# Optimization experiments

Measured on AMD Instinct MI355X. Metric: run time of the kernel, lower is better.

## Reference

```python
import jax, jax.numpy as jnp
import numpy as np

EPS = 1e-12  # F.normalize default eps (denominator = max(norm, eps))


def setup_inputs() -> dict:
    key = jax.random.key(0)
    ks = jax.random.split(key, 8)
    B, FIN, H, W = 4, 256, 64, 64
    N_MEM, SQ = 64, 16           # sqrt_fin = fin**0.5
    POS_CH = 2                    # PosEncoding concatenates one coord channel per dim
    CIN = FIN + POS_CH
    QK = N_MEM * SQ               # 1024
    # PosEncoding buffer: normalized coordinate grid in [-1, 1], shape [2, H, W]
    ys = jnp.linspace(-1.0, 1.0, H, dtype=jnp.float32)
    xs = jnp.linspace(-1.0, 1.0, W, dtype=jnp.float32)
    gy, gx = jnp.meshgrid(ys, xs, indexing='ij')
    pos = jnp.stack([gy, gx], axis=0)
    s = 0.02
    return {
        'x':    jax.random.normal(ks[0], (B, FIN, H, W), jnp.float32),
        'pos':  pos,
        'wq':   jax.random.normal(ks[1], (QK, CIN), jnp.float32) * s,
        'bq':   jnp.zeros((QK,), jnp.float32),
        'wk':   jax.random.normal(ks[2], (QK, CIN), jnp.float32) * s,
        'bk':   jnp.zeros((QK,), jnp.float32),
        'v':    jax.random.normal(ks[3], (N_MEM, FIN), jnp.float32) * s,
        'wout': jax.random.normal(ks[4], (FIN, FIN), jnp.float32) * s,
        'bout': jnp.zeros((FIN,), jnp.float32),
    }


def reference(x, pos, wq, bq, wk, bk, v, wout, bout):
    B, C, H, W = x.shape
    S = H * W
    n_mem, fin = v.shape
    sq = wq.shape[0] // n_mem
    # PosEncoding: concat coordinate channels
    posb = jnp.broadcast_to(pos[None], (B,) + pos.shape)
    xp = jnp.concatenate([x, posb], axis=1).reshape(B, C + pos.shape[0], S)
    # 1x1 conv projections (channel GEMMs)
    q = jnp.einsum('oc,bcs->bos', wq, xp) + bq[None, :, None]  # [B, n_mem*sq, S]
    k = jnp.einsum('oc,bcs->bos', wk, xp) + bk[None, :, None]
    q = q.reshape(B, n_mem, sq, S).transpose(0, 3, 1, 2)  # [B,S,m,sq]
    k = k.reshape(B, n_mem, sq, S).transpose(0, 3, 2, 1)  # [B,S,sq,m]
    # F.normalize: q over last dim (sqrt_fin), k over dim=1 (sqrt_fin)
    qn = q / jnp.maximum(jnp.linalg.norm(q, axis=-1, keepdims=True), EPS)
    kn = k / jnp.maximum(jnp.linalg.norm(k, axis=2, keepdims=True), EPS)
    # attn[b,s,m,n] = qn . kn ; dropout is identity in eval mode.
    # mean over memory slots m commutes with (attn @ v), so fuse:
    attn_mean = jnp.einsum('bsk,bskn->bsn', qn.mean(axis=2), kn)  # [B,S,n_mem]
    mem = attn_mean @ v                                            # [B,S,fin]
    mem = mem.transpose(0, 2, 1).reshape(B, fin, H, W)
    out = jnp.einsum('of,bfhw->bohw', wout, mem) + bout[None, :, None, None]
    return x + out
```

## Files before the change

kernel.cpp:

```cpp
#include <hip/hip_runtime.h>
#include <stdint.h>

#define EPSN 1e-12f

typedef float f32x16 __attribute__((ext_vector_type(16)));
typedef float f32x4 __attribute__((ext_vector_type(4)));
typedef __bf16 bf16x8 __attribute__((ext_vector_type(8)));
typedef long long i64x2 __attribute__((ext_vector_type(2)));

__device__ __forceinline__ unsigned short f2bf(float f) {
  union { float f; unsigned int u; } v; v.f = f;
  unsigned int u = v.u + 0x7FFFu + ((v.u >> 16) & 1u);
  return (unsigned short)(u >> 16);
}

__device__ __forceinline__ unsigned short f2fp8x2(float a, float b) {
  int r = __builtin_amdgcn_cvt_pk_fp8_f32(a, b, 0, false);
  return (unsigned short)(r & 0xFFFF);
}

#define NKS 17
#define WQF_B 0
#define WKF_B (16 * NKS * 64 * 16)
#define WVP_OFF_S (2 * 16 * NKS * 64 * 8)

__global__ __launch_bounds__(256) void prep_kernel(
    const float* __restrict__ wq, const float* __restrict__ bq,
    const float* __restrict__ wk, const float* __restrict__ bk,
    const float* __restrict__ v, const float* __restrict__ wout,
    unsigned short* __restrict__ wsp) {
  uint8_t* wsp8 = (uint8_t*)wsp;
  int bid = blockIdx.x;
  if (bid < 512) {
    int isK = bid >= 256;
    int ob = (bid & 255) * 4;
    const float* w = isK ? wk : wq;
    const float* bb = isK ? bk : bq;
    uint8_t* dst = wsp8 + (isK ? WKF_B : WQF_B);
    for (int i = threadIdx.x; i < 4 * 129; i += 256) {
      int r = i / 129, q = i - r * 129;
      int o = ob + r, k = q * 2;
      float2 w2 = *(const float2*)(w + o * 258 + k);
      int g = o >> 5, col = o & 31, g2 = g >> 1, t = g & 1;
      int ks = k >> 4, hi = (k >> 3) & 1, j = k & 7;
      unsigned short pk = f2fp8x2(w2.x, w2.y);
      *(unsigned short*)(dst +
          (((g2 * NKS + ks) * 64 + hi * 32 + col) << 4) + t * 8 + j) = pk;
    }
    for (int i = threadIdx.x; i < 4 * 14; i += 256) {
      int r = i / 14, kk = 258 + (i - r * 14);
      int o = ob + r;
      int g = o >> 5, col = o & 31, g2 = g >> 1, t = g & 1;
      int ks = kk >> 4, hi = (kk >> 3) & 1, j = kk & 7;
      uint8_t val = (kk == 258) ? (uint8_t)(f2fp8x2(bb[o], 0.f) & 0xFF)
                                : (uint8_t)0;
      dst[(((g2 * NKS + ks) * 64 + hi * 32 + col) << 4) + t * 8 + j] = val;
    }
  } else {
    int idx = (bid - 512) * 256 + threadIdx.x;
    int fc = idx & 15, m = (idx >> 4) & 63, o = idx >> 10;
    const f32x4* wo = (const f32x4*)(wout + o * 256 + fc * 16);
    const f32x4* vm = (const f32x4*)(v + m * 256 + fc * 16);
    float s = 0.f;
#pragma unroll
    for (int f = 0; f < 4; ++f) {
      f32x4 a = wo[f], bvv = vm[f];
      s += a[0]*bvv[0] + a[1]*bvv[1] + a[2]*bvv[2] + a[3]*bvv[3];
    }
    s += __shfl_xor(s, 1, 64);
    s += __shfl_xor(s, 2, 64);
    s += __shfl_xor(s, 4, 64);
    s += __shfl_xor(s, 8, 64);
    if (fc == 0) wsp[WVP_OFF_S + o * 64 + m] = f2bf(s);
  }
}

#define PXB 64
#define KP8 296
#define QS 66
#define AT 72

__global__ __launch_bounds__(1024, 4) void fused_kernel(
    const float* __restrict__ x, const float* __restrict__ pos,
    const unsigned short* __restrict__ wsp, const float* __restrict__ bout,
    float* __restrict__ out) {
  __shared__ __align__(16) uint8_t xp8[PXB * KP8];
  __shared__ __align__(16) float qbarL[16 * QS];
  __shared__ __align__(16) unsigned short attnM[PXB * AT];
  __shared__ float boutL[256];

  const int tid = threadIdx.x;
  const int lane = tid & 63;
  const int wid = __builtin_amdgcn_readfirstlane(tid >> 6);
  const int px = lane & 31, q2 = lane >> 5;
  const int P0 = blockIdx.x * PXB;
  const int b = P0 >> 12, s0 = P0 & 4095;

  const uint8_t* wsp8 = (const uint8_t*)wsp;
  const uint8_t* wqf = wsp8 + WQF_B + wid * (NKS * 1024) + lane * 16;
  const uint8_t* wkf = wsp8 + WKF_B + wid * (NKS * 1024) + lane * 16;

  {
    const float* xrow = x + b * 256 * 4096 + s0;
    f32x4 lo[2], hi[2];
#pragma unroll
    for (int it = 0; it < 2; ++it) {
      int idx = tid + it * 1024;
      int g = idx & 15, dcol = idx >> 4;
      lo[it] = __builtin_nontemporal_load(
          (const f32x4*)(xrow + (2 * dcol) * 4096 + 4 * g));
      hi[it] = __builtin_nontemporal_load(
          (const f32x4*)(xrow + (2 * dcol + 1) * 4096 + 4 * g));
    }
#pragma unroll
    for (int it = 0; it < 2; ++it) {
      int idx = tid + it * 1024;
      int g = idx & 15, dcol = idx >> 4;
#pragma unroll
      for (int j = 0; j < 4; ++j) {
        int pp = 4 * g + j;
        *(unsigned short*)&xp8[pp * KP8 + 2 * dcol] =
            f2fp8x2(lo[it][j], hi[it][j]);
      }
    }
    if (tid < 512) {
      int pp = tid & 63, dcol = 128 + (tid >> 6);
      float t0 = 0.f, t1 = 0.f;
      if (dcol == 128) { t0 = pos[s0 + pp]; t1 = pos[4096 + s0 + pp]; }
      else if (dcol == 129) { t0 = 1.0f; }
      *(unsigned short*)&xp8[pp * KP8 + 2 * dcol] = f2fp8x2(t0, t1);
    }
  }
  if (tid < 256) boutL[tid] = bout[tid];
  for (int i = tid; i < 16 * QS; i += 1024) qbarL[i] = 0.f;
  __syncthreads();

#define PHASE(WB) do {                                                    \
    const uint8_t* _p = (WB);                                             \
    const uint8_t* _b0p = &xp8[px * KP8 + q2 * 8];                        \
    const uint8_t* _b1p = &xp8[(32 + px) * KP8 + q2 * 8];                 \
    i64x2 _Ac = *(const i64x2*)_p;                                        \
    _Pragma("unroll 1")                                                   \
    for (int i = 0; i < NKS - 1; ++i) {                                   \
      i64x2 _An = *(const i64x2*)(_p + (i + 1) * 1024);                   \
      long long _b0 = *(const long long*)(_b0p + i * 16);                 \
      long long _b1 = *(const long long*)(_b1p + i * 16);                 \
      __builtin_amdgcn_s_setprio(1);                                      \
      acc00 = __builtin_amdgcn_mfma_f32_32x32x16_fp8_fp8(_Ac[0], _b0, acc00, 0, 0, 0); \
      acc01 = __builtin_amdgcn_mfma_f32_32x32x16_fp8_fp8(_Ac[0], _b1, acc01, 0, 0, 0); \
      acc10 = __builtin_amdgcn_mfma_f32_32x32x16_fp8_fp8(_Ac[1], _b0, acc10, 0, 0, 0); \
      acc11 = __builtin_amdgcn_mfma_f32_32x32x16_fp8_fp8(_Ac[1], _b1, acc11, 0, 0, 0); \
      __builtin_amdgcn_s_setprio(0);                                      \
      _Ac = _An;                                                          \
    }                                                                     \
    {                                                                     \
      long long _b0 = *(const long long*)(_b0p + (NKS - 1) * 16);         \
      long long _b1 = *(const long long*)(_b1p + (NKS - 1) * 16);         \
      acc00 = __builtin_amdgcn_mfma_f32_32x32x16_fp8_fp8(_Ac[0], _b0, acc00, 0, 0, 0); \
      acc01 = __builtin_amdgcn_mfma_f32_32x32x16_fp8_fp8(_Ac[0], _b1, acc01, 0, 0, 0); \
      acc10 = __builtin_amdgcn_mfma_f32_32x32x16_fp8_fp8(_Ac[1], _b0, acc10, 0, 0, 0); \
      acc11 = __builtin_amdgcn_mfma_f32_32x32x16_fp8_fp8(_Ac[1], _b1, acc11, 0, 0, 0); \
    }                                                                     \
  } while (0)

  f32x16 acc00 = (f32x16)0.f, acc01 = (f32x16)0.f,
         acc10 = (f32x16)0.f, acc11 = (f32x16)0.f;
  PHASE(wqf);

  {
    float qsum[2][8];
#pragma unroll
    for (int nt = 0; nt < 2; ++nt)
#pragma unroll
      for (int r = 0; r < 8; ++r) qsum[nt][r] = 0.f;
#pragma unroll
    for (int ot = 0; ot < 2; ++ot) {
#pragma unroll
      for (int nt = 0; nt < 2; ++nt) {
        const f32x16 a = ot ? (nt ? acc11 : acc10) : (nt ? acc01 : acc00);
        float s20 = 0.f, s21 = 0.f;
#pragma unroll
        for (int r = 0; r < 8; ++r) {
          s20 = fmaf(a[r], a[r], s20);
          s21 = fmaf(a[r + 8], a[r + 8], s21);
        }
        s20 += __shfl_xor(s20, 32, 64);
        s21 += __shfl_xor(s21, 32, 64);
        float i0 = 1.0f / fmaxf(sqrtf(s20), EPSN);
        float i1 = 1.0f / fmaxf(sqrtf(s21), EPSN);
#pragma unroll
        for (int r = 0; r < 8; ++r) qsum[nt][r] += a[r] * i0 + a[r + 8] * i1;
      }
    }
#pragma unroll
    for (int nt = 0; nt < 2; ++nt)
#pragma unroll
      for (int r = 0; r < 8; ++r) {
        int j = (r & 3) + ((r >> 2) << 3) + (q2 << 2);
        atomicAdd(&qbarL[j * QS + nt * 32 + px], qsum[nt][r] * (1.0f / 64.0f));
      }
  }

  acc00 = (f32x16)0.f; acc01 = (f32x16)0.f;
  acc10 = (f32x16)0.f; acc11 = (f32x16)0.f;
  PHASE(wkf);
  __syncthreads();

  {
    float qb[2][8];
#pragma unroll
    for (int nt = 0; nt < 2; ++nt)
#pragma unroll
      for (int r = 0; r < 8; ++r) {
        int j = (r & 3) + ((r >> 2) << 3) + (q2 << 2);
        qb[nt][r] = qbarL[j * QS + nt * 32 + px];
      }
#pragma unroll
    for (int ot = 0; ot < 2; ++ot) {
#pragma unroll
      for (int nt = 0; nt < 2; ++nt) {
        const f32x16 a = ot ? (nt ? acc11 : acc10) : (nt ? acc01 : acc00);
        float s20 = 0.f, s21 = 0.f, sp0 = 0.f, sp1 = 0.f;
#pragma unroll
        for (int r = 0; r < 8; ++r) {
          s20 = fmaf(a[r], a[r], s20);         sp0 = fmaf(qb[nt][r], a[r], sp0);
          s21 = fmaf(a[r + 8], a[r + 8], s21); sp1 = fmaf(qb[nt][r], a[r + 8], sp1);
        }
        s20 += __shfl_xor(s20, 32, 64);
        s21 += __shfl_xor(s21, 32, 64);
        sp0 += __shfl_xor(sp0, 32, 64);
        sp1 += __shfl_xor(sp1, 32, 64);
        if (q2 == 0) {
          int m0 = wid * 4 + ot * 2;
          attnM[(nt * 32 + px) * AT + m0]     = f2bf(sp0 / fmaxf(sqrtf(s20), EPSN));
          attnM[(nt * 32 + px) * AT + m0 + 1] = f2bf(sp1 / fmaxf(sqrtf(s21), EPSN));
        }
      }
    }
  }
  __syncthreads();

  {
    const int otile = wid >> 1, pxt = wid & 1;
    f32x16 e = (f32x16)0.f;
    const unsigned short* wv =
        wsp + WVP_OFF_S + (otile * 32 + px) * 64 + q2 * 8;
    const unsigned short* ab = &attnM[(pxt * 32 + px) * AT + q2 * 8];
#pragma unroll
    for (int ks = 0; ks < 4; ++ks) {
      bf16x8 av = *(const bf16x8*)(wv + ks * 16);
      bf16x8 bv = *(const bf16x8*)(ab + ks * 16);
      e = __builtin_amdgcn_mfma_f32_32x32x16_bf16(av, bv, e, 0, 0, 0);
    }
    const int p = pxt * 32 + px;
#pragma unroll
    for (int r = 0; r < 16; ++r) {
      const int o = otile * 32 + (r & 3) + ((r >> 2) << 3) + (q2 << 2);
      const int gi = (b * 256 + o) * 4096 + s0 + p;
      float xv = __builtin_nontemporal_load(&x[gi]);
      __builtin_nontemporal_store(xv + boutL[o] + e[r], &out[gi]);
    }
  }
#undef PHASE
}

extern "C" void kernel_launch(void* const* d_in, const int* in_sizes, int n_in,
                              void* d_out, int out_size, void* d_ws, size_t ws_size,
                              hipStream_t stream) {
  const float* x    = (const float*)d_in[0];
  const float* pos  = (const float*)d_in[1];
  const float* wq   = (const float*)d_in[2];
  const float* bq   = (const float*)d_in[3];
  const float* wk   = (const float*)d_in[4];
  const float* bk   = (const float*)d_in[5];
  const float* v    = (const float*)d_in[6];
  const float* wout = (const float*)d_in[7];
  const float* bout = (const float*)d_in[8];
  float* out = (float*)d_out;
  unsigned short* wsp = (unsigned short*)d_ws;

  hipLaunchKernelGGL(prep_kernel, dim3(1536), dim3(256), 0, stream,
                     wq, bq, wk, bk, v, wout, wsp);
  hipLaunchKernelGGL(fused_kernel, dim3(256), dim3(1024), 0, stream,
                     x, pos, wsp, bout, out);
}
```

Measured before the change: 127.8 us.

## Switch Q/K projection GEMMs from 32x32x16 to 16x16x32 FP8 MFMA tiles

Replaces the 32x32x16 FP8 MFMA tiling of the fused Q/K projections with a 4x4 grid of 16x16x32 FP8 MFMAs per wave. The prepacked weight layout, its K padding (now 9 steps of 32) and the zero-filled pad columns of the staged activations change to match. The normalisation and attention epilogues now reduce across 16-lane groups instead of 32-lane halves. The aim is a simpler per-row norm epilogue and a different MFMA and register balance. The cost is extra padded K work and more MFMA issues per step.

```diff
diff --git a/kernel.cpp b/kernel.cpp
--- a/kernel.cpp
+++ b/kernel.cpp
@@ -3,8 +3,8 @@
 
 #define EPSN 1e-12f
 
+typedef float f32x4 __attribute__((ext_vector_type(4)));
 typedef float f32x16 __attribute__((ext_vector_type(16)));
-typedef float f32x4 __attribute__((ext_vector_type(4)));
 typedef __bf16 bf16x8 __attribute__((ext_vector_type(8)));
 typedef long long i64x2 __attribute__((ext_vector_type(2)));
 
@@ -19,10 +19,11 @@
   return (unsigned short)(r & 0xFFFF);
 }
 
-#define NKS 17
+#define NKS9 9
+#define GRPB (NKS9 * 64 * 32)
 #define WQF_B 0
-#define WKF_B (16 * NKS * 64 * 16)
-#define WVP_OFF_S (2 * 16 * NKS * 64 * 8)
+#define WKF_B (16 * GRPB)
+#define WVP_OFF_S (2 * 16 * GRPB / 2)
 
 __global__ __launch_bounds__(256) void prep_kernel(
     const float* __restrict__ wq, const float* __restrict__ bq,
@@ -41,20 +42,21 @@
       int r = i / 129, q = i - r * 129;
       int o = ob + r, k = q * 2;
       float2 w2 = *(const float2*)(w + o * 258 + k);
-      int g = o >> 5, col = o & 31, g2 = g >> 1, t = g & 1;
-      int ks = k >> 4, hi = (k >> 3) & 1, j = k & 7;
-      unsigned short pk = f2fp8x2(w2.x, w2.y);
-      *(unsigned short*)(dst +
-          (((g2 * NKS + ks) * 64 + hi * 32 + col) << 4) + t * 8 + j) = pk;
-    }
-    for (int i = threadIdx.x; i < 4 * 14; i += 256) {
-      int r = i / 14, kk = 258 + (i - r * 14);
+      int grp = o >> 6, t = (o >> 4) & 3, r16 = o & 15;
+      int ks = k >> 5, l4 = (k >> 3) & 3, j = k & 7;
+      int lane = l4 * 16 + r16;
+      *(unsigned short*)(dst + ((grp * NKS9 + ks) * 64 + lane) * 32 + t * 8 + j) =
+          f2fp8x2(w2.x, w2.y);
+    }
+    for (int i = threadIdx.x; i < 4 * 30; i += 256) {
+      int r = i / 30, kk = 258 + (i - r * 30);
       int o = ob + r;
-      int g = o >> 5, col = o & 31, g2 = g >> 1, t = g & 1;
-      int ks = kk >> 4, hi = (kk >> 3) & 1, j = kk & 7;
+      int grp = o >> 6, t = (o >> 4) & 3, r16 = o & 15;
+      int ks = kk >> 5, l4 = (kk >> 3) & 3, j = kk & 7;
+      int lane = l4 * 16 + r16;
       uint8_t val = (kk == 258) ? (uint8_t)(f2fp8x2(bb[o], 0.f) & 0xFF)
                                 : (uint8_t)0;
-      dst[(((g2 * NKS + ks) * 64 + hi * 32 + col) << 4) + t * 8 + j] = val;
+      dst[((grp * NKS9 + ks) * 64 + lane) * 32 + t * 8 + j] = val;
     }
   } else {
     int idx = (bid - 512) * 256 + threadIdx.x;
@@ -92,13 +94,13 @@
   const int tid = threadIdx.x;
   const int lane = tid & 63;
   const int wid = __builtin_amdgcn_readfirstlane(tid >> 6);
-  const int px = lane & 31, q2 = lane >> 5;
+  const int l15 = lane & 15, l4 = lane >> 4;
   const int P0 = blockIdx.x * PXB;
   const int b = P0 >> 12, s0 = P0 & 4095;
 
   const uint8_t* wsp8 = (const uint8_t*)wsp;
-  const uint8_t* wqf = wsp8 + WQF_B + wid * (NKS * 1024) + lane * 16;
-  const uint8_t* wkf = wsp8 + WKF_B + wid * (NKS * 1024) + lane * 16;
+  const uint8_t* wqf = wsp8 + WQF_B + wid * GRPB + lane * 32;
+  const uint8_t* wkf = wsp8 + WKF_B + wid * GRPB + lane * 32;
 
   {
     const float* xrow = x + b * 256 * 4096 + s0;
@@ -123,7 +125,7 @@
             f2fp8x2(lo[it][j], hi[it][j]);
       }
     }
-    if (tid < 512) {
+    if (tid < 64 * 20) {
       int pp = tid & 63, dcol = 128 + (tid >> 6);
       float t0 = 0.f, t1 = 0.f;
       if (dcol == 128) { t0 = pos[s0 + pp]; t1 = pos[4096 + s0 + pp]; }
@@ -135,105 +137,118 @@
   for (int i = tid; i < 16 * QS; i += 1024) qbarL[i] = 0.f;
   __syncthreads();
 
+  const uint8_t* bp0 = &xp8[(0 * 16 + l15) * KP8 + l4 * 8];
+  const uint8_t* bp1 = &xp8[(1 * 16 + l15) * KP8 + l4 * 8];
+  const uint8_t* bp2 = &xp8[(2 * 16 + l15) * KP8 + l4 * 8];
+  const uint8_t* bp3 = &xp8[(3 * 16 + l15) * KP8 + l4 * 8];
+
+#define MFMA8(Aop, B, pt) do {                                            \
+    acc[0][pt] = __builtin_amdgcn_mfma_f32_16x16x32_fp8_fp8(Aop[0], B, acc[0][pt], 0, 0, 0); \
+  } while (0)
+
 #define PHASE(WB) do {                                                    \
     const uint8_t* _p = (WB);                                             \
-    const uint8_t* _b0p = &xp8[px * KP8 + q2 * 8];                        \
-    const uint8_t* _b1p = &xp8[(32 + px) * KP8 + q2 * 8];                 \
-    i64x2 _Ac = *(const i64x2*)_p;                                        \
+    i64x2 A0 = *(const i64x2*)(_p);                        \
+    i64x2 A1 = *(const i64x2*)(_p + 16);                   \
     _Pragma("unroll 1")                                                   \
-    for (int i = 0; i < NKS - 1; ++i) {                                   \
-      i64x2 _An = *(const i64x2*)(_p + (i + 1) * 1024);                   \
-      long long _b0 = *(const long long*)(_b0p + i * 16);                 \
-      long long _b1 = *(const long long*)(_b1p + i * 16);                 \
+    for (int i = 0; i < NKS9; ++i) {                                      \
+      i64x2 N0 = A0, N1 = A1;                                             \
+      if (i + 1 < NKS9) {                                                 \
+        N0 = *(const i64x2*)(_p + (i + 1) * 2048);                        \
+        N1 = *(const i64x2*)(_p + (i + 1) * 2048 + 16);                   \
+      }                                                                   \
+      long long b0 = *(const long long*)(bp0 + i * 32);                   \
+      long long b1 = *(const long long*)(bp1 + i * 32);                   \
+      long long b2 = *(const long long*)(bp2 + i * 32);                   \
+      long long b3 = *(const long long*)(bp3 + i * 32);                   \
       __builtin_amdgcn_s_setprio(1);                                      \
-      acc00 = __builtin_amdgcn_mfma_f32_32x32x16_fp8_fp8(_Ac[0], _b0, acc00, 0, 0, 0); \
-      acc01 = __builtin_amdgcn_mfma_f32_32x32x16_fp8_fp8(_Ac[0], _b1, acc01, 0, 0, 0); \
-      acc10 = __builtin_amdgcn_mfma_f32_32x32x16_fp8_fp8(_Ac[1], _b0, acc10, 0, 0, 0); \
-      acc11 = __builtin_amdgcn_mfma_f32_32x32x16_fp8_fp8(_Ac[1], _b1, acc11, 0, 0, 0); \
+      acc[0][0] = __builtin_amdgcn_mfma_f32_16x16x32_fp8_fp8(A0[0], b0, acc[0][0], 0, 0, 0); \
+      acc[0][1] = __builtin_amdgcn_mfma_f32_16x16x32_fp8_fp8(A0[0], b1, acc[0][1], 0, 0, 0); \
+      acc[0][2] = __builtin_amdgcn_mfma_f32_16x16x32_fp8_fp8(A0[0], b2, acc[0][2], 0, 0, 0); \
+      acc[0][3] = __builtin_amdgcn_mfma_f32_16x16x32_fp8_fp8(A0[0], b3, acc[0][3], 0, 0, 0); \
+      acc[1][0] = __builtin_amdgcn_mfma_f32_16x16x32_fp8_fp8(A0[1], b0, acc[1][0], 0, 0, 0); \
+      acc[1][1] = __builtin_amdgcn_mfma_f32_16x16x32_fp8_fp8(A0[1], b1, acc[1][1], 0, 0, 0); \
+      acc[1][2] = __builtin_amdgcn_mfma_f32_16x16x32_fp8_fp8(A0[1], b2, acc[1][2], 0, 0, 0); \
+      acc[1][3] = __builtin_amdgcn_mfma_f32_16x16x32_fp8_fp8(A0[1], b3, acc[1][3], 0, 0, 0); \
+      acc[2][0] = __builtin_amdgcn_mfma_f32_16x16x32_fp8_fp8(A1[0], b0, acc[2][0], 0, 0, 0); \
+      acc[2][1] = __builtin_amdgcn_mfma_f32_16x16x32_fp8_fp8(A1[0], b1, acc[2][1], 0, 0, 0); \
+      acc[2][2] = __builtin_amdgcn_mfma_f32_16x16x32_fp8_fp8(A1[0], b2, acc[2][2], 0, 0, 0); \
+      acc[2][3] = __builtin_amdgcn_mfma_f32_16x16x32_fp8_fp8(A1[0], b3, acc[2][3], 0, 0, 0); \
+      acc[3][0] = __builtin_amdgcn_mfma_f32_16x16x32_fp8_fp8(A1[1], b0, acc[3][0], 0, 0, 0); \
+      acc[3][1] = __builtin_amdgcn_mfma_f32_16x16x32_fp8_fp8(A1[1], b1, acc[3][1], 0, 0, 0); \
+      acc[3][2] = __builtin_amdgcn_mfma_f32_16x16x32_fp8_fp8(A1[1], b2, acc[3][2], 0, 0, 0); \
+      acc[3][3] = __builtin_amdgcn_mfma_f32_16x16x32_fp8_fp8(A1[1], b3, acc[3][3], 0, 0, 0); \
       __builtin_amdgcn_s_setprio(0);                                      \
-      _Ac = _An;                                                          \
-    }                                                                     \
-    {                                                                     \
-      long long _b0 = *(const long long*)(_b0p + (NKS - 1) * 16);         \
-      long long _b1 = *(const long long*)(_b1p + (NKS - 1) * 16);         \
-      acc00 = __builtin_amdgcn_mfma_f32_32x32x16_fp8_fp8(_Ac[0], _b0, acc00, 0, 0, 0); \
-      acc01 = __builtin_amdgcn_mfma_f32_32x32x16_fp8_fp8(_Ac[0], _b1, acc01, 0, 0, 0); \
-      acc10 = __builtin_amdgcn_mfma_f32_32x32x16_fp8_fp8(_Ac[1], _b0, acc10, 0, 0, 0); \
-      acc11 = __builtin_amdgcn_mfma_f32_32x32x16_fp8_fp8(_Ac[1], _b1, acc11, 0, 0, 0); \
+      A0 = N0; A1 = N1;                                                   \
     }                                                                     \
   } while (0)
 
-  f32x16 acc00 = (f32x16)0.f, acc01 = (f32x16)0.f,
-         acc10 = (f32x16)0.f, acc11 = (f32x16)0.f;
+  f32x4 acc[4][4];
+#pragma unroll
+  for (int t = 0; t < 4; ++t)
+#pragma unroll
+    for (int pt = 0; pt < 4; ++pt) acc[t][pt] = (f32x4)0.f;
   PHASE(wqf);
 
   {
-    float qsum[2][8];
-#pragma unroll
-    for (int nt = 0; nt < 2; ++nt)
-#pragma unroll
-      for (int r = 0; r < 8; ++r) qsum[nt][r] = 0.f;
-#pragma unroll
-    for (int ot = 0; ot < 2; ++ot) {
-#pragma unroll
-      for (int nt = 0; nt < 2; ++nt) {
-        const f32x16 a = ot ? (nt ? acc11 : acc10) : (nt ? acc01 : acc00);
-        float s20 = 0.f, s21 = 0.f;
-#pragma unroll
-        for (int r = 0; r < 8; ++r) {
-          s20 = fmaf(a[r], a[r], s20);
-          s21 = fmaf(a[r + 8], a[r + 8], s21);
-        }
-        s20 += __shfl_xor(s20, 32, 64);
-        s21 += __shfl_xor(s21, 32, 64);
-        float i0 = 1.0f / fmaxf(sqrtf(s20), EPSN);
-        float i1 = 1.0f / fmaxf(sqrtf(s21), EPSN);
-#pragma unroll
-        for (int r = 0; r < 8; ++r) qsum[nt][r] += a[r] * i0 + a[r + 8] * i1;
+    float qsum[4][4];
+#pragma unroll
+    for (int pt = 0; pt < 4; ++pt)
+#pragma unroll
+      for (int r = 0; r < 4; ++r) qsum[pt][r] = 0.f;
+#pragma unroll
+    for (int t = 0; t < 4; ++t) {
+#pragma unroll
+      for (int pt = 0; pt < 4; ++pt) {
+        float s2 = 0.f;
+#pragma unroll
+        for (int r = 0; r < 4; ++r) s2 = fmaf(acc[t][pt][r], acc[t][pt][r], s2);
+        s2 += __shfl_xor(s2, 16, 64);
+        s2 += __shfl_xor(s2, 32, 64);
+        float inv = 1.0f / fmaxf(sqrtf(s2), EPSN);
+#pragma unroll
+        for (int r = 0; r < 4; ++r) qsum[pt][r] += acc[t][pt][r] * inv;
       }
     }
 #pragma unroll
-    for (int nt = 0; nt < 2; ++nt)
-#pragma unroll
-      for (int r = 0; r < 8; ++r) {
-        int j = (r & 3) + ((r >> 2) << 3) + (q2 << 2);
-        atomicAdd(&qbarL[j * QS + nt * 32 + px], qsum[nt][r] * (1.0f / 64.0f));
-      }
-  }
-
-  acc00 = (f32x16)0.f; acc01 = (f32x16)0.f;
-  acc10 = (f32x16)0.f; acc11 = (f32x16)0.f;
+    for (int pt = 0; pt < 4; ++pt)
+#pragma unroll
+      for (int r = 0; r < 4; ++r)
+        atomicAdd(&qbarL[(l4 * 4 + r) * QS + pt * 16 + l15],
+                  qsum[pt][r] * (1.0f / 64.0f));
+  }
+
+#pragma unroll
+  for (int t = 0; t < 4; ++t)
+#pragma unroll
+    for (int pt = 0; pt < 4; ++pt) acc[t][pt] = (f32x4)0.f;
   PHASE(wkf);
   __syncthreads();
 
   {
-    float qb[2][8];
-#pragma unroll
-    for (int nt = 0; nt < 2; ++nt)
-#pragma unroll
-      for (int r = 0; r < 8; ++r) {
-        int j = (r & 3) + ((r >> 2) << 3) + (q2 << 2);
-        qb[nt][r] = qbarL[j * QS + nt * 32 + px];
-      }
-#pragma unroll
-    for (int ot = 0; ot < 2; ++ot) {
-#pragma unroll
-      for (int nt = 0; nt < 2; ++nt) {
-        const f32x16 a = ot ? (nt ? acc11 : acc10) : (nt ? acc01 : acc00);
-        float s20 = 0.f, s21 = 0.f, sp0 = 0.f, sp1 = 0.f;
-#pragma unroll
-        for (int r = 0; r < 8; ++r) {
-          s20 = fmaf(a[r], a[r], s20);         sp0 = fmaf(qb[nt][r], a[r], sp0);
-          s21 = fmaf(a[r + 8], a[r + 8], s21); sp1 = fmaf(qb[nt][r], a[r + 8], sp1);
+    float qb[4][4];
+#pragma unroll
+    for (int pt = 0; pt < 4; ++pt)
+#pragma unroll
+      for (int r = 0; r < 4; ++r)
+        qb[pt][r] = qbarL[(l4 * 4 + r) * QS + pt * 16 + l15];
+#pragma unroll
+    for (int t = 0; t < 4; ++t) {
+#pragma unroll
+      for (int pt = 0; pt < 4; ++pt) {
+        float s2 = 0.f, sp = 0.f;
+#pragma unroll
+        for (int r = 0; r < 4; ++r) {
+          s2 = fmaf(acc[t][pt][r], acc[t][pt][r], s2);
+          sp = fmaf(qb[pt][r], acc[t][pt][r], sp);
         }
-        s20 += __shfl_xor(s20, 32, 64);
-        s21 += __shfl_xor(s21, 32, 64);
-        sp0 += __shfl_xor(sp0, 32, 64);
-        sp1 += __shfl_xor(sp1, 32, 64);
-        if (q2 == 0) {
-          int m0 = wid * 4 + ot * 2;
-          attnM[(nt * 32 + px) * AT + m0]     = f2bf(sp0 / fmaxf(sqrtf(s20), EPSN));
-          attnM[(nt * 32 + px) * AT + m0 + 1] = f2bf(sp1 / fmaxf(sqrtf(s21), EPSN));
+        s2 += __shfl_xor(s2, 16, 64);
+        sp += __shfl_xor(sp, 16, 64);
+        s2 += __shfl_xor(s2, 32, 64);
+        sp += __shfl_xor(sp, 32, 64);
+        if (l4 == 0) {
+          attnM[(pt * 16 + l15) * AT + 4 * wid + t] =
+              f2bf(sp / fmaxf(sqrtf(s2), EPSN));
         }
       }
     }
@@ -241,6 +256,7 @@
   __syncthreads();
 
   {
+    const int px = lane & 31, q2 = lane >> 5;
     const int otile = wid >> 1, pxt = wid & 1;
     f32x16 e = (f32x16)0.f;
     const unsigned short* wv =
@@ -262,6 +278,7 @@
     }
   }
 #undef PHASE
+#undef MFMA8
 }
 
 extern "C" void kernel_launch(void* const* d_in, const int* in_sizes, int n_in,
```

Result: slower. 130.4 us (+2.0%).
